# Optimization experiments

Measured on AMD Instinct MI355X. Metric: run time of the kernel, lower is better.

Reference implementation:

```python
import jax, jax.numpy as jnp
import numpy as np

D_MODEL = 1024
H = 16
D_H = D_MODEL // H
B = 8
S = 1024
NEG_INF = -1e9


def setup_inputs() -> dict:
    key = jax.random.key(0)
    ks = jax.random.split(key, 8)
    Qs = jax.random.normal(ks[0], (B, S, D_MODEL), dtype=jnp.float32)
    Ks = jax.random.normal(ks[1], (B, S, D_MODEL), dtype=jnp.float32)
    Vs = jax.random.normal(ks[2], (B, S, D_MODEL), dtype=jnp.float32)
    mask_3d = jnp.zeros((B, S, S), dtype=bool)
    # Parameters: torch.rand -> uniform[0,1) for per-head projections
    W_Q = jax.random.uniform(ks[3], (H, D_MODEL, D_H), dtype=jnp.float32)
    W_K = jax.random.uniform(ks[4], (H, D_MODEL, D_H), dtype=jnp.float32)
    W_V = jax.random.uniform(ks[5], (H, D_MODEL, D_H), dtype=jnp.float32)
    # Output nn.Linear(h*d_h, d_model): weight [d_model, h*d_h], bias [d_model]
    lim = 1.0 / np.sqrt(H * D_H)
    W_out = jax.random.uniform(ks[6], (D_MODEL, H * D_H), minval=-lim, maxval=lim, dtype=jnp.float32)
    b_out = jax.random.uniform(ks[7], (D_MODEL,), minval=-lim, maxval=lim, dtype=jnp.float32)
    return {"Qs": Qs, "Ks": Ks, "Vs": Vs, "mask_3d": mask_3d,
            "W_Q": W_Q, "W_K": W_K, "W_V": W_V, "W_out": W_out, "b_out": b_out}


def reference(Qs, Ks, Vs, mask_3d, W_Q, W_K, W_V, W_out, b_out):
    # Fused per-head projections: avoid the explicit repeat in the torch code.
    q = jnp.einsum('bsk,hkl->bhsl', Qs, W_Q)  # [B,H,S,D_H]
    k = jnp.einsum('bsk,hkl->bhsl', Ks, W_K)
    v = jnp.einsum('bsk,hkl->bhsl', Vs, W_V)
    scale = 1.0 / jnp.sqrt(jnp.asarray(D_H, dtype=q.dtype))
    scores = jnp.einsum('bhqd,bhkd->bhqk', q, k) * scale  # [B,H,S,S]
    scores = jnp.where(mask_3d[:, None, :, :], NEG_INF, scores)
    attn = jax.nn.softmax(scores, axis=-1)
    out = jnp.einsum('bhqk,bhkd->bhqd', attn, v)  # [B,H,S,D_H]
    # chunk along head-batch dim then cat along feature dim == head-major concat
    out = jnp.transpose(out, (0, 2, 1, 3)).reshape(B, S, H * D_H)
    return out @ W_out.T + b_out
```

## Files before the change

kernel.cpp:

```cpp
#include <hip/hip_runtime.h>

#define DM 1024
#define H_ 16
#define DH 64
#define B_ 8
#define S_ 1024

typedef _Float16 half8 __attribute__((ext_vector_type(8)));
typedef _Float16 half4 __attribute__((ext_vector_type(4)));
typedef __fp16 fp16x2 __attribute__((ext_vector_type(2)));
typedef float f32x4 __attribute__((ext_vector_type(4)));
typedef float f32x16 __attribute__((ext_vector_type(16)));
typedef unsigned int uint;

static __device__ __forceinline__ uint pkrtz(float a, float b) {
    fp16x2 h = __builtin_amdgcn_cvt_pkrtz(a, b);
    return __builtin_bit_cast(uint, h);
}
#define PSWAP(d, s) asm volatile("v_permlane32_swap_b32 %0, %1" : "+v"(d), "+v"(s))

static __device__ __forceinline__ void gload16(const _Float16* g, _Float16* l) {
    __builtin_amdgcn_global_load_lds(
        (const __attribute__((address_space(1))) unsigned int*)(const void*)g,
        (__attribute__((address_space(3))) unsigned int*)(void*)l,
        16, 0, 0);
}

__global__ __launch_bounds__(256) void prep_k(
    const float* __restrict__ WQ, const float* __restrict__ WK,
    const float* __restrict__ WV, const float* __restrict__ WO,
    const unsigned char* __restrict__ mask,
    _Float16* __restrict__ wqh, _Float16* __restrict__ wql,
    _Float16* __restrict__ wkh, _Float16* __restrict__ wkl,
    _Float16* __restrict__ wv,  _Float16* __restrict__ wo,
    unsigned char* __restrict__ scan)
{
    __shared__ __align__(16) _Float16 Lh[64][72];
    __shared__ __align__(16) _Float16 Ll[64][72];
    __shared__ int s_red[4];
    const int t = threadIdx.x;
    const int blk = blockIdx.x;

    if (blk < 256) {
        const int kb = blk & 15;
        const int h  = blk >> 4;
        #pragma unroll
        for (int s = 0; s < 3; ++s) {
            const float* W = (s == 0) ? WQ : ((s == 1) ? WK : WV);
            const int krow = t >> 2, lc = t & 3;
            const float* rp = W + (((size_t)h * 1024 + kb * 64 + krow) * 64 + lc * 16);
            #pragma unroll
            for (int q4 = 0; q4 < 4; ++q4) {
                float4 f = ((const float4*)rp)[q4];
                float vv0 = f.x, vv1 = f.y, vv2 = f.z, vv3 = f.w;
                int l0 = lc * 16 + q4 * 4;
                _Float16 h0 = (_Float16)vv0; Lh[l0 + 0][krow] = h0; Ll[l0 + 0][krow] = (_Float16)(vv0 - (float)h0);
                _Float16 h1 = (_Float16)vv1; Lh[l0 + 1][krow] = h1; Ll[l0 + 1][krow] = (_Float16)(vv1 - (float)h1);
                _Float16 h2 = (_Float16)vv2; Lh[l0 + 2][krow] = h2; Ll[l0 + 2][krow] = (_Float16)(vv2 - (float)h2);
                _Float16 h3 = (_Float16)vv3; Lh[l0 + 3][krow] = h3; Ll[l0 + 3][krow] = (_Float16)(vv3 - (float)h3);
            }
            __syncthreads();
            const int l = t >> 2, pc = t & 3;
            #pragma unroll
            for (int hp = 0; hp < 2; ++hp) {
                int p = pc + 4 * hp;
                int lc2 = p ^ (l & 7);
                half8 vh = *(const half8*)&Lh[l][lc2 * 8];
                half8 vl = *(const half8*)&Ll[l][lc2 * 8];
                size_t off = (size_t)(h * 64 + l) * DM + kb * 64 + p * 8;
                if (s == 0) { *(half8*)(wqh + off) = vh; *(half8*)(wql + off) = vl; }
                else if (s == 1) { *(half8*)(wkh + off) = vh; *(half8*)(wkl + off) = vl; }
                else { *(half8*)(wv + off) = vh; }
            }
            __syncthreads();
        }
    } else if (blk < 768) {
        int idx8 = (blk - 256) * 256 + t;
        int n = idx8 >> 7;
        int c = idx8 & 127;
        int p = (c & ~7) | ((c & 7) ^ (n & 7));
        const float* rp = WO + ((size_t)n * DM + c * 8);
        float4 a = ((const float4*)rp)[0];
        float4 b = ((const float4*)rp)[1];
        half8 v;
        v[0] = (_Float16)a.x; v[1] = (_Float16)a.y; v[2] = (_Float16)a.z; v[3] = (_Float16)a.w;
        v[4] = (_Float16)b.x; v[5] = (_Float16)b.y; v[6] = (_Float16)b.z; v[7] = (_Float16)b.w;
        *(half8*)(wo + (size_t)n * DM + p * 8) = v;
    } else {
        const int g = blk - 768;
        const int q64 = g & 15, k64 = (g >> 4) & 15, b = g >> 8;
        uint4 mv = *(const uint4*)(mask + ((size_t)b * S_ + q64 * 64 + (t >> 2)) * S_ + k64 * 64 + (t & 3) * 16);
        int a = (mv.x | mv.y | mv.z | mv.w) != 0;
        unsigned long long bal = __ballot(a);
        if ((t & 63) == 0) s_red[t >> 6] = (bal != 0ull);
        __syncthreads();
        if (t == 0)
            scan[(b * 16 + q64) * 16 + k64] =
                (unsigned char)(s_red[0] | s_red[1] | s_red[2] | s_red[3]);
    }
}

__global__ __launch_bounds__(512) void gemm_split_k(
    const float* __restrict__ A0, const float* __restrict__ A1,
    const _Float16* __restrict__ Bh0, const _Float16* __restrict__ Bl0,
    const _Float16* __restrict__ Bh1, const _Float16* __restrict__ Bl1,
    _Float16* __restrict__ Chi0, _Float16* __restrict__ Clo0,
    _Float16* __restrict__ Chi1, _Float16* __restrict__ Clo1)
{
    const int lid = blockIdx.x + 8 * blockIdx.y + 512 * blockIdx.z;
    const int xcd = lid & 7, k2 = lid >> 3;
    const int G = xcd * 16 + (k2 >> 3);
    const int bxv = k2 & 7, byv = G & 63, z = G >> 6;

    const float* A = z ? A1 : A0;
    const _Float16* Bh = z ? Bh1 : Bh0;
    const _Float16* Bl = z ? Bl1 : Bl0;
    _Float16* Chi = z ? Chi1 : Chi0;
    _Float16* Clo = z ? Clo1 : Clo0;

    __shared__ __align__(16) _Float16 SM[32768];
    _Float16* Ah  = SM;
    _Float16* Al  = SM + 8192;
    _Float16* Bhs = SM + 16384;
    _Float16* Bls = SM + 24576;

    const int t = threadIdx.x;
    const int lane = t & 63;
    const int w = t >> 6;
    const int wm = (w >> 1) * 32;
    const int wn = (w & 1) * 64;
    const int l15 = lane & 15;
    const int l4g = lane >> 4;

    const int bm = byv * 128;
    const int bn = bxv * 128;

    f32x4 acc[2][4] = {};

    float4 ar[4];
    auto aload = [&](int KT) {
        #pragma unroll
        for (int i = 0; i < 4; ++i)
            ar[i] = *(const float4*)(A + (size_t)(bm + (t >> 4) + 32 * i) * DM + KT * 64 + (t & 15) * 4);
    };
    auto awr = [&]() {
        #pragma unroll
        for (int i = 0; i < 4; ++i) {
            int row = (t >> 4) + 32 * i;
            int c4 = t & 15;
            float4 v = ar[i];
            half4 hv, lv;
            hv[0] = (_Float16)v.x; lv[0] = (_Float16)(v.x - (float)hv[0]);
            hv[1] = (_Float16)v.y; lv[1] = (_Float16)(v.y - (float)hv[1]);
            hv[2] = (_Float16)v.z; lv[2] = (_Float16)(v.z - (float)hv[2]);
            hv[3] = (_Float16)v.w; lv[3] = (_Float16)(v.w - (float)hv[3]);
            int off = row * 64 + (((c4 >> 1) ^ (row & 7)) * 8) + (c4 & 1) * 4;
            *(half4*)&Ah[off] = hv;
            *(half4*)&Al[off] = lv;
        }
    };
    auto bgl = [&](int KT) {
        #pragma unroll
        for (int jj = 0; jj < 2; ++jj) {
            int rr = w * 16 + jj * 8 + (lane >> 3);
            const size_t so = (size_t)(bn + rr) * DM + KT * 64 + (lane & 7) * 8;
            gload16(Bh + so, &Bhs[(w * 16 + jj * 8) * 64]);
            gload16(Bl + so, &Bls[(w * 16 + jj * 8) * 64]);
        }
    };

    aload(0);
    bgl(0);
    for (int kt = 0; kt < 16; ++kt) {
        awr();
        __syncthreads();
        if (kt < 15) aload(kt + 1);
        #pragma unroll
        for (int ks = 0; ks < 2; ++ks) {
            half8 ah[2], al[2], bh[4], bl[4];
            const int slotx = (ks * 4 + l4g);
            #pragma unroll
            for (int mi = 0; mi < 2; ++mi) {
                int r = wm + mi * 16 + l15;
                int off = r * 64 + (slotx ^ (l15 & 7)) * 8;
                ah[mi] = *(const half8*)&Ah[off];
                al[mi] = *(const half8*)&Al[off];
            }
            #pragma unroll
            for (int ni = 0; ni < 4; ++ni) {
                int r = wn + ni * 16 + l15;
                int off = r * 64 + (slotx ^ (l15 & 7)) * 8;
                bh[ni] = *(const half8*)&Bhs[off];
                bl[ni] = *(const half8*)&Bls[off];
            }
            #pragma unroll
            for (int mi = 0; mi < 2; ++mi)
                #pragma unroll
                for (int ni = 0; ni < 4; ++ni) {
                    acc[mi][ni] = __builtin_amdgcn_mfma_f32_16x16x32_f16(ah[mi], bh[ni], acc[mi][ni], 0, 0, 0);
                    acc[mi][ni] = __builtin_amdgcn_mfma_f32_16x16x32_f16(ah[mi], bl[ni], acc[mi][ni], 0, 0, 0);
                    acc[mi][ni] = __builtin_amdgcn_mfma_f32_16x16x32_f16(al[mi], bh[ni], acc[mi][ni], 0, 0, 0);
                }
        }
        __syncthreads();
        if (kt < 15) bgl(kt + 1);
    }

    #pragma unroll
    for (int mi = 0; mi < 2; ++mi)
        #pragma unroll
        for (int ni = 0; ni < 4; ++ni) {
            int col = bn + wn + ni * 16 + l15;
            #pragma unroll
            for (int r = 0; r < 4; ++r) {
                int row = bm + wm + mi * 16 + l4g * 4 + r;
                float val = acc[mi][ni][r];
                _Float16 hv = (_Float16)val;
                Chi[(size_t)row * DM + col] = hv;
                Clo[(size_t)row * DM + col] = (_Float16)(val - (float)hv);
            }
        }
}

__global__ __launch_bounds__(256) void gemm_v_k(
    const float* __restrict__ A, const _Float16* __restrict__ Bt,
    _Float16* __restrict__ C)
{
    const int lid = blockIdx.x + 8 * blockIdx.y;
    const int xcd = lid & 7, k2 = lid >> 3;
    const int G = xcd * 8 + (k2 >> 3);
    const int bxv = k2 & 7, byv = G;

    __shared__ __align__(16) _Float16 SM[25600];
    _Float16* As  = SM;
    _Float16* Bsb = SM + 9216;

    const int t = threadIdx.x;
    const int lane = t & 63;
    const int w = t >> 6;
    const int wm = (w >> 1) * 64;
    const int wn = (w & 1) * 64;
    const int l15 = lane & 15;
    const int l4g = lane >> 4;

    const int bm = byv * 128;
    const int bn = bxv * 128;

    f32x4 acc[4][4] = {};

    const int arow = t >> 4, ac4 = t & 15;
    float4 ar[8];
    auto aload = [&](int KT) {
        #pragma unroll
        for (int i = 0; i < 8; ++i)
            ar[i] = *(const float4*)(A + (size_t)(bm + arow + 16 * i) * DM + KT * 64 + ac4 * 4);
    };
    auto awr = [&]() {
        #pragma unroll
        for (int i = 0; i < 8; ++i) {
            float4 v = ar[i];
            half4 hv;
            hv[0] = (_Float16)v.x; hv[1] = (_Float16)v.y;
            hv[2] = (_Float16)v.z; hv[3] = (_Float16)v.w;
            *(half4*)&As[(arow + 16 * i) * 72 + ac4 * 4] = hv;
        }
    };
    auto bgl = [&](int KT, int buf) {
        _Float16* Bd = Bsb + buf * 8192;
        #pragma unroll
        for (int jj = 0; jj < 4; ++jj) {
            int rr = w * 32 + jj * 8 + (lane >> 3);
            gload16(Bt + (size_t)(bn + rr) * DM + KT * 64 + (lane & 7) * 8,
                    &Bd[(w * 32 + jj * 8) * 64]);
        }
    };

    aload(0);
    bgl(0, 0);
    for (int kt = 0; kt < 16; ++kt) {
        const _Float16* Bcur = Bsb + (kt & 1) * 8192;
        awr();
        __syncthreads();
        if (kt < 15) { aload(kt + 1); bgl(kt + 1, (kt + 1) & 1); }
        #pragma unroll
        for (int ks = 0; ks < 2; ++ks) {
            half8 a[4], b[4];
            #pragma unroll
            for (int mi = 0; mi < 4; ++mi)
                a[mi] = *(const half8*)&As[(wm + mi * 16 + l15) * 72 + ks * 32 + l4g * 8];
            #pragma unroll
            for (int ni = 0; ni < 4; ++ni) {
                int row = wn + ni * 16 + l15;
                int slot = (ks * 4 + l4g) ^ (l15 & 7);
                b[ni] = *(const half8*)&Bcur[row * 64 + slot * 8];
            }
            #pragma unroll
            for (int mi = 0; mi < 4; ++mi)
                #pragma unroll
                for (int ni = 0; ni < 4; ++ni)
                    acc[mi][ni] = __builtin_amdgcn_mfma_f32_16x16x32_f16(a[mi], b[ni], acc[mi][ni], 0, 0, 0);
        }
        __syncthreads();
    }

    _Float16* Tw = SM + w * 4608;
    #pragma unroll
    for (int mi = 0; mi < 4; ++mi)
        #pragma unroll
        for (int ni = 0; ni < 4; ++ni)
            #pragma unroll
            for (int r = 0; r < 4; ++r)
                Tw[(ni * 16 + l15) * 72 + mi * 16 + l4g * 4 + r] = (_Float16)acc[mi][ni][r];
    __syncthreads();
    {
        const int mg0 = bm + wm;
        const int b = mg0 >> 10, s0 = mg0 & 1023;
        _Float16* op = C + ((size_t)b * DM + (bn + wn + lane)) * S_ + s0;
        #pragma unroll
        for (int c8 = 0; c8 < 8; ++c8)
            *(half8*)(op + c8 * 8) = *(const half8*)&Tw[lane * 72 + c8 * 8];
    }
}

__global__ __launch_bounds__(256) void gemm_out_k(
    const _Float16* __restrict__ A, const _Float16* __restrict__ Bt,
    float* __restrict__ C, const float* __restrict__ bias)
{
    const int lid = blockIdx.x + 8 * blockIdx.y;
    const int xcd = lid & 7, k2 = lid >> 3;
    const int G = xcd * 8 + (k2 >> 3);
    const int bxv = k2 & 7, byv = G;

    __shared__ __align__(16) _Float16 SM[32768];

    const int t = threadIdx.x;
    const int lane = t & 63;
    const int w = t >> 6;
    const int wm = (w >> 1) * 64;
    const int wn = (w & 1) * 64;
    const int l15 = lane & 15;
    const int l4g = lane >> 4;

    const int bm = byv * 128;
    const int bn = bxv * 128;

    f32x4 acc[4][4] = {};

    auto stage = [&](int KT, int buf) {
        _Float16* Ad = SM + buf * 8192;
        _Float16* Bd = SM + 16384 + buf * 8192;
        #pragma unroll
        for (int jj = 0; jj < 4; ++jj) {
            int rr = w * 32 + jj * 8 + (lane >> 3);
            const size_t go = (size_t)rr * DM + KT * 64 + (lane & 7) * 8;
            gload16(A + (size_t)bm * DM + go, Ad + (w * 32 + jj * 8) * 64);
            gload16(Bt + (size_t)bn * DM + go, Bd + (w * 32 + jj * 8) * 64);
        }
    };

    stage(0, 0);
    __syncthreads();
    for (int kt = 0; kt < 16; ++kt) {
        const int buf = kt & 1;
        if (kt < 15) stage(kt + 1, buf ^ 1);
        const _Float16* Ac = SM + buf * 8192;
        const _Float16* Bc = SM + 16384 + buf * 8192;
        #pragma unroll
        for (int ks = 0; ks < 2; ++ks) {
            half8 a[4], b[4];
            const int slotx = ks * 4 + l4g;
            #pragma unroll
            for (int mi = 0; mi < 4; ++mi) {
                int row = wm + mi * 16 + l15;
                a[mi] = *(const half8*)&Ac[row * 64 + ((slotx ^ (l15 & 7)) * 8)];
            }
            #pragma unroll
            for (int ni = 0; ni < 4; ++ni) {
                int row = wn + ni * 16 + l15;
                b[ni] = *(const half8*)&Bc[row * 64 + ((slotx ^ (l15 & 7)) * 8)];
            }
            #pragma unroll
            for (int mi = 0; mi < 4; ++mi)
                #pragma unroll
                for (int ni = 0; ni < 4; ++ni)
                    acc[mi][ni] = __builtin_amdgcn_mfma_f32_16x16x32_f16(a[mi], b[ni], acc[mi][ni], 0, 0, 0);
        }
        __syncthreads();
    }

    #pragma unroll
    for (int mi = 0; mi < 4; ++mi)
        #pragma unroll
        for (int ni = 0; ni < 4; ++ni) {
            int col = bn + wn + ni * 16 + l15;
            #pragma unroll
            for (int r = 0; r < 4; ++r) {
                int row = bm + wm + mi * 16 + l4g * 4 + r;
                C[(size_t)row * DM + col] = acc[mi][ni][r] + bias[col];
            }
        }
}

__global__ __launch_bounds__(256) void attn_k(
    const _Float16* __restrict__ qhg, const _Float16* __restrict__ qlg,
    const _Float16* __restrict__ khg, const _Float16* __restrict__ klg,
    const _Float16* __restrict__ vtg, const unsigned char* __restrict__ maskg,
    const unsigned char* __restrict__ scanp, _Float16* __restrict__ ho)
{
    __shared__ __align__(16) _Float16 KhB[2][64][72];
    __shared__ __align__(16) _Float16 KlB[2][64][72];
    __shared__ __align__(16) _Float16 VtB[2][64][72];

    const int t = threadIdx.x;
    const int lane = t & 63;
    const int w = t >> 6;
    const int l31 = lane & 31;
    const int hi = lane >> 5;

    const int j = blockIdx.y + 16 * blockIdx.z;
    const int head = 16 * blockIdx.x + (j >> 3);
    const int qt = j & 7;
    const int h = head & 15;
    const int b = head >> 4;

    const int colbase = h * DH;
    const int qrow = qt * 128 + w * 32 + l31;

    half8 qfh[4], qfl[4];
    {
        const size_t base = ((size_t)b * S_ + qrow) * DM + colbase;
        #pragma unroll
        for (int ds = 0; ds < 4; ++ds) {
            qfh[ds] = *(const half8*)(qhg + base + ds * 16 + hi * 8);
            qfl[ds] = *(const half8*)(qlg + base + ds * 16 + hi * 8);
        }
    }

    float m_q = -1e30f, ls = 0.0f;
    f32x16 accO0 = {};
    f32x16 accO1 = {};

    const int r0 = t >> 3;
    const int c0 = (t & 7) * 8;
    const _Float16* kph = khg + ((size_t)b * S_) * DM + colbase;
    const _Float16* kpl = klg + ((size_t)b * S_) * DM + colbase;
    const _Float16* vp  = vtg + ((size_t)b * DM + colbase) * S_;
    const unsigned char* sc0 = scanp + (b * 16 + 2 * qt) * 16;
    const unsigned char* sc1 = scanp + (b * 16 + 2 * qt + 1) * 16;

    uint4 akh0, akh1, akl0, akl1, av0, av1;
#define ALOAD(KT) do { \
        akh0 = *(const uint4*)(kph + (size_t)((KT) * 64 + r0) * DM + c0);       \
        akh1 = *(const uint4*)(kph + (size_t)((KT) * 64 + 32 + r0) * DM + c0);  \
        akl0 = *(const uint4*)(kpl + (size_t)((KT) * 64 + r0) * DM + c0);       \
        akl1 = *(const uint4*)(kpl + (size_t)((KT) * 64 + 32 + r0) * DM + c0);  \
        av0  = *(const uint4*)(vp + (size_t)r0 * S_ + (KT) * 64 + c0);          \
        av1  = *(const uint4*)(vp + (size_t)(32 + r0) * S_ + (KT) * 64 + c0);   \
    } while (0)
#define AWRITE(BUF) do { \
        *(uint4*)&KhB[BUF][r0][c0] = akh0; *(uint4*)&KhB[BUF][32 + r0][c0] = akh1; \
        *(uint4*)&KlB[BUF][r0][c0] = akl0; *(uint4*)&KlB[BUF][32 + r0][c0] = akl1; \
        *(uint4*)&VtB[BUF][r0][c0] = av0;  *(uint4*)&VtB[BUF][32 + r0][c0] = av1;  \
    } while (0)

    ALOAD(0);
    AWRITE(0);
    int msk = sc0[0] | sc1[0];

    const float SC = 0.125f * 1.44269504089f;
    const float THRRAW = 8.0f / SC;

    for (int kt = 0; kt < 16; ++kt) {
        __syncthreads();
        const int cur = kt & 1;
        const int mskcur = msk;
        if (kt < 15) {
            ALOAD(kt + 1);
            msk = sc0[kt + 1] | sc1[kt + 1];
        }

        f32x16 sa0 = {}, sa1 = {};
        __builtin_amdgcn_s_setprio(1);
        #pragma unroll
        for (int ds = 0; ds < 4; ++ds) {
            half8 kh0 = *(const half8*)&KhB[cur][l31][ds * 16 + hi * 8];
            half8 kl0 = *(const half8*)&KlB[cur][l31][ds * 16 + hi * 8];
            half8 kh1 = *(const half8*)&KhB[cur][32 + l31][ds * 16 + hi * 8];
            half8 kl1 = *(const half8*)&KlB[cur][32 + l31][ds * 16 + hi * 8];
            sa0 = __builtin_amdgcn_mfma_f32_32x32x16_f16(kh0, qfh[ds], sa0, 0, 0, 0);
            sa0 = __builtin_amdgcn_mfma_f32_32x32x16_f16(kh0, qfl[ds], sa0, 0, 0, 0);
            sa0 = __builtin_amdgcn_mfma_f32_32x32x16_f16(kl0, qfh[ds], sa0, 0, 0, 0);
            sa1 = __builtin_amdgcn_mfma_f32_32x32x16_f16(kh1, qfh[ds], sa1, 0, 0, 0);
            sa1 = __builtin_amdgcn_mfma_f32_32x32x16_f16(kh1, qfl[ds], sa1, 0, 0, 0);
            sa1 = __builtin_amdgcn_mfma_f32_32x32x16_f16(kl1, qfh[ds], sa1, 0, 0, 0);
        }
        __builtin_amdgcn_s_setprio(0);

        if (mskcur) {
            const unsigned char* mrow = maskg + ((size_t)b * S_ + qrow) * S_ + kt * 64;
            #pragma unroll
            for (int e = 0; e < 16; ++e) {
                int kl_ = (e & 3) + 8 * (e >> 2) + 4 * hi;
                if (mrow[kl_]) sa0[e] = -1e9f;
                if (mrow[32 + kl_]) sa1[e] = -1e9f;
            }
        }

        float rm = fmaxf(sa0[0], sa0[1]);
        #pragma unroll
        for (int e = 2; e < 16; e += 2) rm = fmaxf(fmaxf(rm, sa0[e]), sa0[e + 1]);
        #pragma unroll
        for (int e = 0; e < 16; e += 2) rm = fmaxf(fmaxf(rm, sa1[e]), sa1[e + 1]);
        rm = fmaxf(rm, __shfl_xor(rm, 32));
        if (__any(rm > m_q + THRRAW)) {
            const float mn = fmaxf(m_q, rm);
            const float sfac = exp2f((m_q - mn) * SC);
            m_q = mn;
            ls *= sfac;
            #pragma unroll
            for (int e = 0; e < 16; ++e) { accO0[e] *= sfac; accO1[e] *= sfac; }
        }
        const float nmn = -m_q * SC;
        float rs = 0.0f;
        #pragma unroll
        for (int e = 0; e < 16; ++e) { sa0[e] = exp2f(fmaf(sa0[e], SC, nmn)); rs += sa0[e]; }
        #pragma unroll
        for (int e = 0; e < 16; ++e) { sa1[e] = exp2f(fmaf(sa1[e], SC, nmn)); rs += sa1[e]; }
        rs += __shfl_xor(rs, 32);
        ls += rs;

        half8 pf[4];
        {
            uint c0_ = pkrtz(sa0[0], sa0[1]),  c1_ = pkrtz(sa0[2], sa0[3]);
            uint c2_ = pkrtz(sa0[4], sa0[5]),  c3_ = pkrtz(sa0[6], sa0[7]);
            uint c4_ = pkrtz(sa0[8], sa0[9]),  c5_ = pkrtz(sa0[10], sa0[11]);
            uint c6_ = pkrtz(sa0[12], sa0[13]), c7_ = pkrtz(sa0[14], sa0[15]);
            PSWAP(c0_, c2_); PSWAP(c1_, c3_);
            PSWAP(c4_, c6_); PSWAP(c5_, c7_);
            uint4 u0 = {c0_, c1_, c2_, c3_}, u1 = {c4_, c5_, c6_, c7_};
            pf[0] = __builtin_bit_cast(half8, u0);
            pf[1] = __builtin_bit_cast(half8, u1);
        }
        {
            uint c0_ = pkrtz(sa1[0], sa1[1]),  c1_ = pkrtz(sa1[2], sa1[3]);
            uint c2_ = pkrtz(sa1[4], sa1[5]),  c3_ = pkrtz(sa1[6], sa1[7]);
            uint c4_ = pkrtz(sa1[8], sa1[9]),  c5_ = pkrtz(sa1[10], sa1[11]);
            uint c6_ = pkrtz(sa1[12], sa1[13]), c7_ = pkrtz(sa1[14], sa1[15]);
            PSWAP(c0_, c2_); PSWAP(c1_, c3_);
            PSWAP(c4_, c6_); PSWAP(c5_, c7_);
            uint4 u0 = {c0_, c1_, c2_, c3_}, u1 = {c4_, c5_, c6_, c7_};
            pf[2] = __builtin_bit_cast(half8, u0);
            pf[3] = __builtin_bit_cast(half8, u1);
        }
        __builtin_amdgcn_s_setprio(1);
        #pragma unroll
        for (int kc = 0; kc < 4; ++kc) {
            half8 vf0 = *(const half8*)&VtB[cur][l31][kc * 16 + hi * 8];
            half8 vf1 = *(const half8*)&VtB[cur][32 + l31][kc * 16 + hi * 8];
            accO0 = __builtin_amdgcn_mfma_f32_32x32x16_f16(vf0, pf[kc], accO0, 0, 0, 0);
            accO1 = __builtin_amdgcn_mfma_f32_32x32x16_f16(vf1, pf[kc], accO1, 0, 0, 0);
        }
        __builtin_amdgcn_s_setprio(0);

        if (kt < 15) AWRITE(cur ^ 1);
    }
#undef ALOAD
#undef AWRITE

    const float inv = 1.0f / ls;
    _Float16* orow = ho + ((size_t)b * S_ + qrow) * DM + colbase;
    const int key = qrow & 7;
    #pragma unroll
    for (int g2 = 0; g2 < 4; ++g2) {
        half4 hv0, hv1;
        #pragma unroll
        for (int e = 0; e < 4; ++e) {
            hv0[e] = (_Float16)(accO0[g2 * 4 + e] * inv);
            hv1[e] = (_Float16)(accO1[g2 * 4 + e] * inv);
        }
        *(half4*)(orow + (g2 ^ key) * 8 + hi * 4) = hv0;
        *(half4*)(orow + ((4 + g2) ^ key) * 8 + hi * 4) = hv1;
    }
}

extern "C" void kernel_launch(void* const* d_in, const int* in_sizes, int n_in,
                              void* d_out, int out_size, void* d_ws, size_t ws_size,
                              hipStream_t stream)
{
    const float* Qs = (const float*)d_in[0];
    const float* Ks = (const float*)d_in[1];
    const float* Vs = (const float*)d_in[2];
    const unsigned char* mask = (const unsigned char*)d_in[3];
    const float* WQ = (const float*)d_in[4];
    const float* WK = (const float*)d_in[5];
    const float* WV = (const float*)d_in[6];
    const float* WO = (const float*)d_in[7];
    const float* bo = (const float*)d_in[8];

    char* ws = (char*)d_ws;
    const size_t MB = 1024 * 1024;
    _Float16* wqh = (_Float16*)(ws + 0 * MB);
    _Float16* wql = (_Float16*)(ws + 2 * MB);
    _Float16* wkh = (_Float16*)(ws + 4 * MB);
    _Float16* wkl = (_Float16*)(ws + 6 * MB);
    _Float16* wv  = (_Float16*)(ws + 8 * MB);
    _Float16* wo  = (_Float16*)(ws + 10 * MB);
    _Float16* qhi = (_Float16*)(ws + 12 * MB);
    _Float16* qlo = (_Float16*)(ws + 28 * MB);
    _Float16* khi = (_Float16*)(ws + 44 * MB);
    _Float16* klo = (_Float16*)(ws + 60 * MB);
    _Float16* vt  = (_Float16*)(ws + 76 * MB);
    _Float16* hh  = (_Float16*)(ws + 92 * MB);
    unsigned char* scan = (unsigned char*)(ws + 108 * MB);

    prep_k<<<2816, 256, 0, stream>>>(WQ, WK, WV, WO, mask,
                                     wqh, wql, wkh, wkl, wv, wo, scan);

    gemm_split_k<<<dim3(8, 64, 2), 512, 0, stream>>>(
        Qs, Ks, wqh, wql, wkh, wkl, qhi, qlo, khi, klo);

    gemm_v_k<<<dim3(8, 64), 256, 0, stream>>>(Vs, wv, vt);

    attn_k<<<dim3(8, 16, 8), 256, 0, stream>>>(qhi, qlo, khi, klo, vt, mask, scan, hh);

    gemm_out_k<<<dim3(8, 64), 256, 0, stream>>>(hh, wo, (float*)d_out, bo);
}
```

Measured before the change: 268.3 us.

## Fuse V projection GEMM into the split Q/K projection kernel launch

```diff
diff --git a/kernel.cpp b/kernel.cpp
--- a/kernel.cpp
+++ b/kernel.cpp
@@ -100,29 +100,16 @@
     }
 }
 
-__global__ __launch_bounds__(512) void gemm_split_k(
-    const float* __restrict__ A0, const float* __restrict__ A1,
+__global__ __launch_bounds__(512) void gemm_qkv_k(
+    const float* __restrict__ A0, const float* __restrict__ A1, const float* __restrict__ A2,
     const _Float16* __restrict__ Bh0, const _Float16* __restrict__ Bl0,
     const _Float16* __restrict__ Bh1, const _Float16* __restrict__ Bl1,
+    const _Float16* __restrict__ Bv,
     _Float16* __restrict__ Chi0, _Float16* __restrict__ Clo0,
-    _Float16* __restrict__ Chi1, _Float16* __restrict__ Clo1)
+    _Float16* __restrict__ Chi1, _Float16* __restrict__ Clo1,
+    _Float16* __restrict__ Cv)
 {
-    const int lid = blockIdx.x + 8 * blockIdx.y + 512 * blockIdx.z;
-    const int xcd = lid & 7, k2 = lid >> 3;
-    const int G = xcd * 16 + (k2 >> 3);
-    const int bxv = k2 & 7, byv = G & 63, z = G >> 6;
-
-    const float* A = z ? A1 : A0;
-    const _Float16* Bh = z ? Bh1 : Bh0;
-    const _Float16* Bl = z ? Bl1 : Bl0;
-    _Float16* Chi = z ? Chi1 : Chi0;
-    _Float16* Clo = z ? Clo1 : Clo0;
-
     __shared__ __align__(16) _Float16 SM[32768];
-    _Float16* Ah  = SM;
-    _Float16* Al  = SM + 8192;
-    _Float16* Bhs = SM + 16384;
-    _Float16* Bls = SM + 24576;
 
     const int t = threadIdx.x;
     const int lane = t & 63;
@@ -132,193 +119,205 @@
     const int l15 = lane & 15;
     const int l4g = lane >> 4;
 
-    const int bm = byv * 128;
-    const int bn = bxv * 128;
-
-    f32x4 acc[2][4] = {};
-
-    float4 ar[4];
-    auto aload = [&](int KT) {
-        #pragma unroll
-        for (int i = 0; i < 4; ++i)
-            ar[i] = *(const float4*)(A + (size_t)(bm + (t >> 4) + 32 * i) * DM + KT * 64 + (t & 15) * 4);
-    };
-    auto awr = [&]() {
-        #pragma unroll
-        for (int i = 0; i < 4; ++i) {
-            int row = (t >> 4) + 32 * i;
-            int c4 = t & 15;
-            float4 v = ar[i];
-            half4 hv, lv;
-            hv[0] = (_Float16)v.x; lv[0] = (_Float16)(v.x - (float)hv[0]);
-            hv[1] = (_Float16)v.y; lv[1] = (_Float16)(v.y - (float)hv[1]);
-            hv[2] = (_Float16)v.z; lv[2] = (_Float16)(v.z - (float)hv[2]);
-            hv[3] = (_Float16)v.w; lv[3] = (_Float16)(v.w - (float)hv[3]);
-            int off = row * 64 + (((c4 >> 1) ^ (row & 7)) * 8) + (c4 & 1) * 4;
-            *(half4*)&Ah[off] = hv;
-            *(half4*)&Al[off] = lv;
-        }
-    };
-    auto bgl = [&](int KT) {
-        #pragma unroll
-        for (int jj = 0; jj < 2; ++jj) {
-            int rr = w * 16 + jj * 8 + (lane >> 3);
-            const size_t so = (size_t)(bn + rr) * DM + KT * 64 + (lane & 7) * 8;
-            gload16(Bh + so, &Bhs[(w * 16 + jj * 8) * 64]);
-            gload16(Bl + so, &Bls[(w * 16 + jj * 8) * 64]);
-        }
-    };
-
-    aload(0);
-    bgl(0);
-    for (int kt = 0; kt < 16; ++kt) {
-        awr();
+    const int lid = blockIdx.x + 8 * blockIdx.y + 512 * blockIdx.z;
+
+    if (lid < 1024) {
+        const int xcd = lid & 7, k2 = lid >> 3;
+        const int G = xcd * 16 + (k2 >> 3);
+        const int bxv = k2 & 7, byv = G & 63, z = G >> 6;
+
+        const float* A = z ? A1 : A0;
+        const _Float16* Bh = z ? Bh1 : Bh0;
+        const _Float16* Bl = z ? Bl1 : Bl0;
+        _Float16* Chi = z ? Chi1 : Chi0;
+        _Float16* Clo = z ? Clo1 : Clo0;
+
+        _Float16* Ah  = SM;
+        _Float16* Al  = SM + 8192;
+        _Float16* Bhs = SM + 16384;
+        _Float16* Bls = SM + 24576;
+
+        const int bm = byv * 128;
+        const int bn = bxv * 128;
+
+        f32x4 acc[2][4] = {};
+
+        float4 ar[4];
+        auto aload = [&](int KT) {
+            #pragma unroll
+            for (int i = 0; i < 4; ++i)
+                ar[i] = *(const float4*)(A + (size_t)(bm + (t >> 4) + 32 * i) * DM + KT * 64 + (t & 15) * 4);
+        };
+        auto awr = [&]() {
+            #pragma unroll
+            for (int i = 0; i < 4; ++i) {
+                int row = (t >> 4) + 32 * i;
+                int c4 = t & 15;
+                float4 v = ar[i];
+                half4 hv, lv;
+                hv[0] = (_Float16)v.x; lv[0] = (_Float16)(v.x - (float)hv[0]);
+                hv[1] = (_Float16)v.y; lv[1] = (_Float16)(v.y - (float)hv[1]);
+                hv[2] = (_Float16)v.z; lv[2] = (_Float16)(v.z - (float)hv[2]);
+                hv[3] = (_Float16)v.w; lv[3] = (_Float16)(v.w - (float)hv[3]);
+                int off = row * 64 + (((c4 >> 1) ^ (row & 7)) * 8) + (c4 & 1) * 4;
+                *(half4*)&Ah[off] = hv;
+                *(half4*)&Al[off] = lv;
+            }
+        };
+        auto bgl = [&](int KT) {
+            #pragma unroll
+            for (int jj = 0; jj < 2; ++jj) {
+                int rr = w * 16 + jj * 8 + (lane >> 3);
+                const size_t so = (size_t)(bn + rr) * DM + KT * 64 + (lane & 7) * 8;
+                gload16(Bh + so, &SM[16384 + (w * 16 + jj * 8) * 64]);
+                gload16(Bl + so, &SM[24576 + (w * 16 + jj * 8) * 64]);
+            }
+        };
+
+        aload(0);
+        bgl(0);
+        for (int kt = 0; kt < 16; ++kt) {
+            awr();
+            __syncthreads();
+            if (kt < 15) aload(kt + 1);
+            #pragma unroll
+            for (int ks = 0; ks < 2; ++ks) {
+                half8 ah[2], al[2], bh[4], bl[4];
+                const int slotx = (ks * 4 + l4g);
+                #pragma unroll
+                for (int mi = 0; mi < 2; ++mi) {
+                    int r = wm + mi * 16 + l15;
+                    int off = r * 64 + (slotx ^ (l15 & 7)) * 8;
+                    ah[mi] = *(const half8*)&Ah[off];
+                    al[mi] = *(const half8*)&Al[off];
+                }
+                #pragma unroll
+                for (int ni = 0; ni < 4; ++ni) {
+                    int r = wn + ni * 16 + l15;
+                    int off = r * 64 + (slotx ^ (l15 & 7)) * 8;
+                    bh[ni] = *(const half8*)&Bhs[off];
+                    bl[ni] = *(const half8*)&Bls[off];
+                }
+                #pragma unroll
+                for (int mi = 0; mi < 2; ++mi)
+                    #pragma unroll
+                    for (int ni = 0; ni < 4; ++ni) {
+                        acc[mi][ni] = __builtin_amdgcn_mfma_f32_16x16x32_f16(ah[mi], bh[ni], acc[mi][ni], 0, 0, 0);
+                        acc[mi][ni] = __builtin_amdgcn_mfma_f32_16x16x32_f16(ah[mi], bl[ni], acc[mi][ni], 0, 0, 0);
+                        acc[mi][ni] = __builtin_amdgcn_mfma_f32_16x16x32_f16(al[mi], bh[ni], acc[mi][ni], 0, 0, 0);
+                    }
+            }
+            __syncthreads();
+            if (kt < 15) bgl(kt + 1);
+        }
+
+        #pragma unroll
+        for (int mi = 0; mi < 2; ++mi)
+            #pragma unroll
+            for (int ni = 0; ni < 4; ++ni) {
+                int col = bn + wn + ni * 16 + l15;
+                #pragma unroll
+                for (int r = 0; r < 4; ++r) {
+                    int row = bm + wm + mi * 16 + l4g * 4 + r;
+                    float val = acc[mi][ni][r];
+                    _Float16 hv = (_Float16)val;
+                    Chi[(size_t)row * DM + col] = hv;
+                    Clo[(size_t)row * DM + col] = (_Float16)(val - (float)hv);
+                }
+            }
+    } else {
+        const int lid2 = lid - 1024;
+        const int xcd = lid2 & 7, k2 = lid2 >> 3;
+        const int G = xcd * 8 + (k2 >> 3);
+        const int bxv = k2 & 7, byv = G;
+
+        _Float16* Ah  = SM;
+        _Float16* Bhs = SM + 16384;
+
+        const int bm = byv * 128;
+        const int bn = bxv * 128;
+
+        f32x4 acc[2][4] = {};
+
+        float4 ar[4];
+        auto aload = [&](int KT) {
+            #pragma unroll
+            for (int i = 0; i < 4; ++i)
+                ar[i] = *(const float4*)(A2 + (size_t)(bm + (t >> 4) + 32 * i) * DM + KT * 64 + (t & 15) * 4);
+        };
+        auto awr = [&]() {
+            #pragma unroll
+            for (int i = 0; i < 4; ++i) {
+                int row = (t >> 4) + 32 * i;
+                int c4 = t & 15;
+                float4 v = ar[i];
+                half4 hv;
+                hv[0] = (_Float16)v.x; hv[1] = (_Float16)v.y;
+                hv[2] = (_Float16)v.z; hv[3] = (_Float16)v.w;
+                int off = row * 64 + (((c4 >> 1) ^ (row & 7)) * 8) + (c4 & 1) * 4;
+                *(half4*)&Ah[off] = hv;
+            }
+        };
+        auto bgl = [&](int KT) {
+            #pragma unroll
+            for (int jj = 0; jj < 2; ++jj) {
+                int rr = w * 16 + jj * 8 + (lane >> 3);
+                gload16(Bv + (size_t)(bn + rr) * DM + KT * 64 + (lane & 7) * 8,
+                        &SM[16384 + (w * 16 + jj * 8) * 64]);
+            }
+        };
+
+        aload(0);
+        bgl(0);
+        for (int kt = 0; kt < 16; ++kt) {
+            awr();
+            __syncthreads();
+            if (kt < 15) aload(kt + 1);
+            #pragma unroll
+            for (int ks = 0; ks < 2; ++ks) {
+                half8 a[2], b[4];
+                const int slotx = (ks * 4 + l4g);
+                #pragma unroll
+                for (int mi = 0; mi < 2; ++mi) {
+                    int r = wm + mi * 16 + l15;
+                    a[mi] = *(const half8*)&Ah[r * 64 + (slotx ^ (l15 & 7)) * 8];
+                }
+                #pragma unroll
+                for (int ni = 0; ni < 4; ++ni) {
+                    int r = wn + ni * 16 + l15;
+                    b[ni] = *(const half8*)&Bhs[r * 64 + (slotx ^ (l15 & 7)) * 8];
+                }
+                #pragma unroll
+                for (int mi = 0; mi < 2; ++mi)
+                    #pragma unroll
+                    for (int ni = 0; ni < 4; ++ni)
+                        acc[mi][ni] = __builtin_amdgcn_mfma_f32_16x16x32_f16(a[mi], b[ni], acc[mi][ni], 0, 0, 0);
+            }
+            __syncthreads();
+            if (kt < 15) bgl(kt + 1);
+        }
+
+        _Float16* Tw = SM + w * 2176;
         __syncthreads();
-        if (kt < 15) aload(kt + 1);
-        #pragma unroll
-        for (int ks = 0; ks < 2; ++ks) {
-            half8 ah[2], al[2], bh[4], bl[4];
-            const int slotx = (ks * 4 + l4g);
-            #pragma unroll
-            for (int mi = 0; mi < 2; ++mi) {
-                int r = wm + mi * 16 + l15;
-                int off = r * 64 + (slotx ^ (l15 & 7)) * 8;
-                ah[mi] = *(const half8*)&Ah[off];
-                al[mi] = *(const half8*)&Al[off];
-            }
+        #pragma unroll
+        for (int mi = 0; mi < 2; ++mi)
             #pragma unroll
             for (int ni = 0; ni < 4; ++ni) {
-                int r = wn + ni * 16 + l15;
-                int off = r * 64 + (slotx ^ (l15 & 7)) * 8;
-                bh[ni] = *(const half8*)&Bhs[off];
-                bl[ni] = *(const half8*)&Bls[off];
-            }
-            #pragma unroll
-            for (int mi = 0; mi < 2; ++mi)
-                #pragma unroll
-                for (int ni = 0; ni < 4; ++ni) {
-                    acc[mi][ni] = __builtin_amdgcn_mfma_f32_16x16x32_f16(ah[mi], bh[ni], acc[mi][ni], 0, 0, 0);
-                    acc[mi][ni] = __builtin_amdgcn_mfma_f32_16x16x32_f16(ah[mi], bl[ni], acc[mi][ni], 0, 0, 0);
-                    acc[mi][ni] = __builtin_amdgcn_mfma_f32_16x16x32_f16(al[mi], bh[ni], acc[mi][ni], 0, 0, 0);
-                }
-        }
+                half4 hv;
+                #pragma unroll
+                for (int r = 0; r < 4; ++r)
+                    hv[r] = (_Float16)acc[mi][ni][r];
+                *(half4*)&Tw[(ni * 16 + l15) * 34 + mi * 16 + l4g * 4] = hv;
+            }
         __syncthreads();
-        if (kt < 15) bgl(kt + 1);
-    }
-
-    #pragma unroll
-    for (int mi = 0; mi < 2; ++mi)
-        #pragma unroll
-        for (int ni = 0; ni < 4; ++ni) {
-            int col = bn + wn + ni * 16 + l15;
-            #pragma unroll
-            for (int r = 0; r < 4; ++r) {
-                int row = bm + wm + mi * 16 + l4g * 4 + r;
-                float val = acc[mi][ni][r];
-                _Float16 hv = (_Float16)val;
-                Chi[(size_t)row * DM + col] = hv;
-                Clo[(size_t)row * DM + col] = (_Float16)(val - (float)hv);
-            }
-        }
-}
-
-__global__ __launch_bounds__(256) void gemm_v_k(
-    const float* __restrict__ A, const _Float16* __restrict__ Bt,
-    _Float16* __restrict__ C)
-{
-    const int lid = blockIdx.x + 8 * blockIdx.y;
-    const int xcd = lid & 7, k2 = lid >> 3;
-    const int G = xcd * 8 + (k2 >> 3);
-    const int bxv = k2 & 7, byv = G;
-
-    __shared__ __align__(16) _Float16 SM[25600];
-    _Float16* As  = SM;
-    _Float16* Bsb = SM + 9216;
-
-    const int t = threadIdx.x;
-    const int lane = t & 63;
-    const int w = t >> 6;
-    const int wm = (w >> 1) * 64;
-    const int wn = (w & 1) * 64;
-    const int l15 = lane & 15;
-    const int l4g = lane >> 4;
-
-    const int bm = byv * 128;
-    const int bn = bxv * 128;
-
-    f32x4 acc[4][4] = {};
-
-    const int arow = t >> 4, ac4 = t & 15;
-    float4 ar[8];
-    auto aload = [&](int KT) {
-        #pragma unroll
-        for (int i = 0; i < 8; ++i)
-            ar[i] = *(const float4*)(A + (size_t)(bm + arow + 16 * i) * DM + KT * 64 + ac4 * 4);
-    };
-    auto awr = [&]() {
-        #pragma unroll
-        for (int i = 0; i < 8; ++i) {
-            float4 v = ar[i];
-            half4 hv;
-            hv[0] = (_Float16)v.x; hv[1] = (_Float16)v.y;
-            hv[2] = (_Float16)v.z; hv[3] = (_Float16)v.w;
-            *(half4*)&As[(arow + 16 * i) * 72 + ac4 * 4] = hv;
-        }
-    };
-    auto bgl = [&](int KT, int buf) {
-        _Float16* Bd = Bsb + buf * 8192;
-        #pragma unroll
-        for (int jj = 0; jj < 4; ++jj) {
-            int rr = w * 32 + jj * 8 + (lane >> 3);
-            gload16(Bt + (size_t)(bn + rr) * DM + KT * 64 + (lane & 7) * 8,
-                    &Bd[(w * 32 + jj * 8) * 64]);
-        }
-    };
-
-    aload(0);
-    bgl(0, 0);
-    for (int kt = 0; kt < 16; ++kt) {
-        const _Float16* Bcur = Bsb + (kt & 1) * 8192;
-        awr();
-        __syncthreads();
-        if (kt < 15) { aload(kt + 1); bgl(kt + 1, (kt + 1) & 1); }
-        #pragma unroll
-        for (int ks = 0; ks < 2; ++ks) {
-            half8 a[4], b[4];
-            #pragma unroll
-            for (int mi = 0; mi < 4; ++mi)
-                a[mi] = *(const half8*)&As[(wm + mi * 16 + l15) * 72 + ks * 32 + l4g * 8];
-            #pragma unroll
-            for (int ni = 0; ni < 4; ++ni) {
-                int row = wn + ni * 16 + l15;
-                int slot = (ks * 4 + l4g) ^ (l15 & 7);
-                b[ni] = *(const half8*)&Bcur[row * 64 + slot * 8];
-            }
-            #pragma unroll
-            for (int mi = 0; mi < 4; ++mi)
-                #pragma unroll
-                for (int ni = 0; ni < 4; ++ni)
-                    acc[mi][ni] = __builtin_amdgcn_mfma_f32_16x16x32_f16(a[mi], b[ni], acc[mi][ni], 0, 0, 0);
-        }
-        __syncthreads();
-    }
-
-    _Float16* Tw = SM + w * 4608;
-    #pragma unroll
-    for (int mi = 0; mi < 4; ++mi)
-        #pragma unroll
-        for (int ni = 0; ni < 4; ++ni)
-            #pragma unroll
-            for (int r = 0; r < 4; ++r)
-                Tw[(ni * 16 + l15) * 72 + mi * 16 + l4g * 4 + r] = (_Float16)acc[mi][ni][r];
-    __syncthreads();
-    {
-        const int mg0 = bm + wm;
-        const int b = mg0 >> 10, s0 = mg0 & 1023;
-        _Float16* op = C + ((size_t)b * DM + (bn + wn + lane)) * S_ + s0;
-        #pragma unroll
-        for (int c8 = 0; c8 < 8; ++c8)
-            *(half8*)(op + c8 * 8) = *(const half8*)&Tw[lane * 72 + c8 * 8];
+        {
+            const int mg0 = bm + wm;
+            const int b = mg0 >> 10, s0 = mg0 & 1023;
+            _Float16* op = Cv + ((size_t)b * DM + (bn + wn + lane)) * S_ + s0;
+            #pragma unroll
+            for (int c8 = 0; c8 < 4; ++c8)
+                *(half8*)(op + c8 * 8) = *(const half8*)&Tw[lane * 34 + c8 * 8];
+        }
     }
 }
 
@@ -616,10 +615,9 @@
     prep_k<<<2816, 256, 0, stream>>>(WQ, WK, WV, WO, mask,
                                      wqh, wql, wkh, wkl, wv, wo, scan);
 
-    gemm_split_k<<<dim3(8, 64, 2), 512, 0, stream>>>(
-        Qs, Ks, wqh, wql, wkh, wkl, qhi, qlo, khi, klo);
-
-    gemm_v_k<<<dim3(8, 64), 256, 0, stream>>>(Vs, wv, vt);
+    gemm_qkv_k<<<dim3(8, 64, 3), 512, 0, stream>>>(
+        Qs, Ks, Vs, wqh, wql, wkh, wkl, wv,
+        qhi, qlo, khi, klo, vt);
 
     attn_k<<<dim3(8, 16, 8), 256, 0, stream>>>(qhi, qlo, khi, klo, vt, mask, scan, hh);
 
```

Result: faster. 261.7 us, median of 2 (-2.5%).
